# Kernel tuning notes

Hardware: AMD Instinct MI355X
Metric: run time of the kernel (lower is better)

The kernel has to match this reference:

```python
import jax, jax.numpy as jnp
from jax import lax
import numpy as np

GAMMA = 1e-4  # RBF bandwidth (init kwarg gamma)

def setup_inputs() -> dict:
    key = jax.random.key(0)
    ks = jax.random.split(key, 6)
    B, H, W = 2048, 64, 64
    P, D = 4096, 4096  # D = 4 * (H//2) * (W//2)
    NC = 10
    x = jax.random.normal(ks[0], (B, 1, H, W), dtype=jnp.float32)
    prototypes = jax.random.normal(ks[1], (P, D), dtype=jnp.float32) * 0.5
    conv_w = jax.random.normal(ks[2], (4, 1, 2, 2), dtype=jnp.float32) * 0.5
    conv_b = jax.random.normal(ks[3], (4,), dtype=jnp.float32) * 0.1
    head_w = jax.random.normal(ks[4], (NC, P), dtype=jnp.float32) * (1.0 / np.sqrt(P))
    head_b = jax.random.normal(ks[5], (NC,), dtype=jnp.float32) * 0.1
    return {"x": x, "prototypes": prototypes, "conv_w": conv_w,
            "conv_b": conv_b, "head_w": head_w, "head_b": head_b}

def reference(x, prototypes, conv_w, conv_b, head_w, head_b):
    # 2x2 stride-2 conv: [B,1,H,W] -> [B,4,H/2,W/2]
    feats = lax.conv_general_dilated(
        x, conv_w, window_strides=(2, 2), padding="VALID",
        dimension_numbers=("NCHW", "OIHW", "NCHW"))
    feats = feats + conv_b[None, :, None, None]
    B = feats.shape[0]
    feats = feats.reshape(B, -1)  # [B, D]
    # Pairwise squared distance via ||f||^2 + ||p||^2 - 2 f.p (no [B,P,D] blowup)
    f2 = jnp.sum(feats * feats, axis=1, keepdims=True)          # [B,1]
    p2 = jnp.sum(prototypes * prototypes, axis=1)[None, :]      # [1,P]
    d2 = jnp.maximum(f2 + p2 - 2.0 * feats @ prototypes.T, 0.0)  # [B,P]
    kernel_vals = jnp.exp(-GAMMA * d2)
    logits = kernel_vals @ head_w.T + head_b
    return jax.nn.log_softmax(logits, axis=-1)
```

## Files before the change

### kernel.cpp

```cpp
#include <hip/hip_runtime.h>
#include <hip/hip_bf16.h>
#include <stdint.h>

#define GAMMA 1e-4f

typedef int i32x4 __attribute__((ext_vector_type(4)));
typedef int i32x8 __attribute__((ext_vector_type(8)));
typedef float f32x4 __attribute__((ext_vector_type(4)));

__device__ __forceinline__ float bf2f(unsigned short u) {
  unsigned int x = ((unsigned int)u) << 16;
  float f; __builtin_memcpy(&f, &x, 4);
  return f;
}

__device__ __forceinline__ unsigned char f2e4m3(float x) {
  float a = fabsf(x);
  unsigned char s = x < 0.f ? 0x80 : 0;
  a = fminf(a, 448.f);
  if (a < 0.015625f) {
    int q = (int)rintf(a * 512.f);
    return s | (unsigned char)q;
  }
  unsigned int u; __builtin_memcpy(&u, &a, 4);
  u += 0x7FFFFu + ((u >> 20) & 1);
  u &= 0xFFF00000u;
  int e2 = (int)(u >> 23) - 127;
  unsigned int mant = (u >> 20) & 7;
  return s | (unsigned char)(((e2 + 7) << 3) | mant);
}

__device__ __forceinline__ unsigned int pack4(float a, float b, float c, float d) {
  return (unsigned)f2e4m3(a) | ((unsigned)f2e4m3(b) << 8) |
         ((unsigned)f2e4m3(c) << 16) | ((unsigned)f2e4m3(d) << 24);
}

__global__ __launch_bounds__(256) void prep_k(
    const float* __restrict__ x, const float* __restrict__ cw,
    const float* __restrict__ cb, unsigned char* __restrict__ fA8,
    float* __restrict__ f2, const float* __restrict__ pr,
    unsigned char* __restrict__ pB8, float* __restrict__ p2) {
  const int tid = threadIdx.x;
  __shared__ float red[4];
  if (blockIdx.x < 4096) {
    const int j = blockIdx.x;
    const float4* src = (const float4*)(pr + (size_t)j * 4096);
    float ssq = 0.f;
    unsigned int w4[4];
#pragma unroll
    for (int k = 0; k < 4; k++) {
      float4 v = src[tid * 4 + k];
      ssq += v.x * v.x + v.y * v.y + v.z * v.z + v.w * v.w;
      w4[k] = pack4(v.x, v.y, v.z, v.w);
    }
    *(uint4*)(pB8 + (size_t)j * 4096 + tid * 16) = make_uint4(w4[0], w4[1], w4[2], w4[3]);
    for (int off = 32; off > 0; off >>= 1) ssq += __shfl_down(ssq, off);
    if ((tid & 63) == 0) red[tid >> 6] = ssq;
    __syncthreads();
    if (tid == 0) p2[j] = red[0] + red[1] + red[2] + red[3];
  } else {
    const int b = blockIdx.x - 4096;
    __shared__ float swb[20];
    if (tid < 16) swb[tid] = cw[tid];
    else if (tid < 20) swb[tid] = cb[tid - 16];
    __syncthreads();
    float w[16], bias[4];
#pragma unroll
    for (int i = 0; i < 16; i++) w[i] = swb[i];
#pragma unroll
    for (int c = 0; c < 4; c++) bias[c] = swb[16 + c];
    const float* xb = x + (size_t)b * 4096;
    unsigned char* fb8 = fA8 + (size_t)b * 4096;
    const int p0 = tid * 4;
    const int h = p0 >> 5, w0 = p0 & 31;
    const float* r0 = xb + (2 * h) * 64 + 2 * w0;
    const float* r1 = r0 + 64;
    float4 a0 = *(const float4*)r0, a1 = *(const float4*)(r0 + 4);
    float4 c0 = *(const float4*)r1, c1 = *(const float4*)(r1 + 4);
    float ssq = 0.f;
#pragma unroll
    for (int c = 0; c < 4; c++) {
      float w00 = w[c * 4], w01 = w[c * 4 + 1], w10 = w[c * 4 + 2], w11 = w[c * 4 + 3];
      float v0 = bias[c] + a0.x * w00 + a0.y * w01 + c0.x * w10 + c0.y * w11;
      float v1 = bias[c] + a0.z * w00 + a0.w * w01 + c0.z * w10 + c0.w * w11;
      float v2 = bias[c] + a1.x * w00 + a1.y * w01 + c1.x * w10 + c1.y * w11;
      float v3 = bias[c] + a1.z * w00 + a1.w * w01 + c1.z * w10 + c1.w * w11;
      ssq += v0 * v0 + v1 * v1 + v2 * v2 + v3 * v3;
      *(unsigned int*)(fb8 + c * 1024 + p0) = pack4(v0, v1, v2, v3);
    }
    for (int off = 32; off > 0; off >>= 1) ssq += __shfl_down(ssq, off);
    if ((tid & 63) == 0) red[tid >> 6] = ssq;
    __syncthreads();
    if (tid == 0) f2[b] = red[0] + red[1] + red[2] + red[3];
  }
}

#define SWZA(o) ((o) ^ ((((o) >> 12) & 1) << 4))
#define SWZB(o) ((o) ^ ((((o) >> 13) & 1) << 4))
#define TILE_BYTES 49152

#define GLDS(gsrc, ldst)                                                    \
  __builtin_amdgcn_global_load_lds(                                         \
      (__attribute__((address_space(1))) void*)(void*)(gsrc),               \
      (__attribute__((address_space(3))) void*)(ldst), 16, 0, 0)

#define MFMA8(a, b, c)                                                      \
  __builtin_amdgcn_mfma_scale_f32_16x16x128_f8f6f4(                         \
      (a), (b), (c), 0, 0, 0, 0x7f7f7f7fu, 0, 0x7f7f7f7fu)

__device__ __forceinline__ i32x8 read32(const char* p0, const char* p1) {
  i32x4 lo = *(const i32x4*)p0;
  i32x4 hi = *(const i32x4*)p1;
  return __builtin_shufflevector(lo, hi, 0, 1, 2, 3, 4, 5, 6, 7);
}

#define TILE_BODY(PT, DO_STAGE, KB, VMWAIT_CODE)                            \
  {                                                                         \
    i32x8 av0, av1, av2, av3, bv0, bv1, bv2, bv3;                           \
    __builtin_amdgcn_sched_barrier(0);                                      \
    av0 = read32((PT) + arlo[0], (PT) + arhi[0]);                           \
    av1 = read32((PT) + arlo[1], (PT) + arhi[1]);                           \
    av2 = read32((PT) + arlo[2], (PT) + arhi[2]);                           \
    av3 = read32((PT) + arlo[3], (PT) + arhi[3]);                           \
    bv0 = read32((PT) + brlo[0], (PT) + brhi[0]);                           \
    bv1 = read32((PT) + brlo[1], (PT) + brhi[1]);                           \
    __builtin_amdgcn_sched_barrier(0);                                      \
    if (DO_STAGE) {                                                         \
      GLDS(agp[0] + (KB), pt2 + aoff[0]);                                   \
      GLDS(agp[1] + (KB), pt2 + aoff[1]);                                   \
      GLDS(bgp[0] + (KB), pt2 + 16384 + boff[0]);                           \
    }                                                                       \
    bv2 = read32((PT) + brlo[2], (PT) + brhi[2]);                           \
    bv3 = read32((PT) + brlo[3], (PT) + brhi[3]);                           \
    if (DO_STAGE) {                                                         \
      GLDS(bgp[1] + (KB), pt2 + 16384 + boff[1]);                           \
      GLDS(bgp[2] + (KB), pt2 + 16384 + boff[2]);                           \
      GLDS(bgp[3] + (KB), pt2 + 16384 + boff[3]);                           \
    }                                                                       \
    __builtin_amdgcn_sched_barrier(0);                                      \
    asm volatile("s_waitcnt lgkmcnt(4)" ::: "memory");                      \
    __builtin_amdgcn_sched_barrier(0);                                      \
    __builtin_amdgcn_s_setprio(1);                                          \
    acc[0][0] = MFMA8(av0, bv0, acc[0][0]);                                 \
    acc[0][1] = MFMA8(av0, bv1, acc[0][1]);                                 \
    acc[1][0] = MFMA8(av1, bv0, acc[1][0]);                                 \
    acc[1][1] = MFMA8(av1, bv1, acc[1][1]);                                 \
    acc[2][0] = MFMA8(av2, bv0, acc[2][0]);                                 \
    acc[2][1] = MFMA8(av2, bv1, acc[2][1]);                                 \
    acc[3][0] = MFMA8(av3, bv0, acc[3][0]);                                 \
    acc[3][1] = MFMA8(av3, bv1, acc[3][1]);                                 \
    __builtin_amdgcn_s_setprio(0);                                          \
    __builtin_amdgcn_sched_barrier(0);                                      \
    asm volatile("s_waitcnt lgkmcnt(0)" ::: "memory");                      \
    __builtin_amdgcn_sched_barrier(0);                                      \
    __builtin_amdgcn_s_setprio(1);                                          \
    acc[0][2] = MFMA8(av0, bv2, acc[0][2]);                                 \
    acc[0][3] = MFMA8(av0, bv3, acc[0][3]);                                 \
    acc[1][2] = MFMA8(av1, bv2, acc[1][2]);                                 \
    acc[1][3] = MFMA8(av1, bv3, acc[1][3]);                                 \
    acc[2][2] = MFMA8(av2, bv2, acc[2][2]);                                 \
    acc[2][3] = MFMA8(av2, bv3, acc[2][3]);                                 \
    acc[3][2] = MFMA8(av3, bv2, acc[3][2]);                                 \
    acc[3][3] = MFMA8(av3, bv3, acc[3][3]);                                 \
    __builtin_amdgcn_s_setprio(0);                                          \
    VMWAIT_CODE;                                                            \
    __builtin_amdgcn_sched_barrier(0);                                      \
  }

__global__ __launch_bounds__(512, 1) void gemm_kv_k(
    const unsigned char* __restrict__ A, const unsigned char* __restrict__ B,
    const float* __restrict__ f2, const float* __restrict__ p2,
    __hip_bfloat16* __restrict__ kv) {
  __shared__ __align__(16) char lds[3 * TILE_BYTES];
  const int tid = threadIdx.x;
  const int wave = tid >> 6, lane = tid & 63;
  const int q = lane >> 4, l16 = lane & 15;
  const int wr = wave >> 2, wc = wave & 3;

  const int wg = blockIdx.x;
  const int xcd = wg & 7, loc = wg >> 3;
  const int bm = (xcd & 1) * 8 + (loc & 7);
  const int bn = (xcd >> 1) * 4 + (loc >> 3);

  const unsigned char* agp[2];
  const unsigned char* bgp[4];
  int aoff[2], boff[4];
#pragma unroll
  for (int i = 0; i < 2; i++) {
    int phys = (tid + i * 512) * 16;
    aoff[i] = phys;
    int lg = SWZA(phys);
    int kq = lg >> 12, rw = (lg & 4095) >> 5, kl = lg & 31;
    agp[i] = A + (size_t)(bm * 128 + rw) * 4096 + kq * 32 + kl;
  }
#pragma unroll
  for (int i = 0; i < 4; i++) {
    int phys = (tid + i * 512) * 16;
    boff[i] = phys;
    int lg = SWZB(phys);
    int kq = lg >> 13, rw = (lg & 8191) >> 5, kl = lg & 31;
    bgp[i] = B + (size_t)(bn * 256 + rw) * 4096 + kq * 32 + kl;
  }

  int arlo[4], arhi[4], brlo[4], brhi[4];
#pragma unroll
  for (int m = 0; m < 4; m++) {
    int lg = q * 4096 + (wr * 64 + m * 16 + l16) * 32;
    arlo[m] = SWZA(lg);
    arhi[m] = SWZA(lg + 16);
  }
#pragma unroll
  for (int n = 0; n < 4; n++) {
    int lg = q * 8192 + (wc * 64 + n * 16 + l16) * 32;
    brlo[n] = 16384 + SWZB(lg);
    brhi[n] = 16384 + SWZB(lg + 16);
  }

  f32x4 acc[4][4] = {};

  char* pt0 = lds;
  char* pt1 = lds + TILE_BYTES;
  char* pt2 = lds + 2 * TILE_BYTES;

#pragma unroll
  for (int i = 0; i < 2; i++) GLDS(agp[i], pt0 + aoff[i]);
#pragma unroll
  for (int i = 0; i < 4; i++) GLDS(bgp[i], pt0 + 16384 + boff[i]);
#pragma unroll
  for (int i = 0; i < 2; i++) GLDS(agp[i] + 128, pt1 + aoff[i]);
#pragma unroll
  for (int i = 0; i < 4; i++) GLDS(bgp[i] + 128, pt1 + 16384 + boff[i]);
  asm volatile("s_waitcnt vmcnt(6)" ::: "memory");
  __builtin_amdgcn_s_barrier();

#pragma unroll 1
  for (int t = 0; t < 30; ++t) {
    const size_t kb2 = (size_t)(t + 2) * 128;
    TILE_BODY(pt0, 1, kb2,
              asm volatile("s_waitcnt vmcnt(6)" ::: "memory");
              __builtin_amdgcn_sched_barrier(0);
              __builtin_amdgcn_s_barrier());
    char* tmp = pt0; pt0 = pt1; pt1 = pt2; pt2 = tmp;
  }
  TILE_BODY(pt0, 0, 0,
            asm volatile("s_waitcnt vmcnt(0)" ::: "memory");
            __builtin_amdgcn_sched_barrier(0);
            __builtin_amdgcn_s_barrier());
  pt0 = pt1;
  TILE_BODY(pt0, 0, 0, );

  float p2v[4];
#pragma unroll
  for (int n = 0; n < 4; n++) p2v[n] = p2[bn * 256 + wc * 64 + n * 16 + l16];
#pragma unroll
  for (int m = 0; m < 4; m++) {
#pragma unroll
    for (int j = 0; j < 4; j++) {
      int grow = bm * 128 + wr * 64 + m * 16 + q * 4 + j;
      float f2v = f2[grow];
      __hip_bfloat16* kvp = kv + (size_t)grow * 4096 + bn * 256 + wc * 64 + l16;
#pragma unroll
      for (int n = 0; n < 4; n++) {
        float d2 = fmaxf(f2v + p2v[n] - 2.0f * acc[m][n][j], 0.f);
        kvp[n * 16] = __float2bfloat16(__expf(-GAMMA * d2));
      }
    }
  }
}

__global__ __launch_bounds__(256) void head_ls_k(
    const __hip_bfloat16* __restrict__ kv, const float* __restrict__ hw,
    const float* __restrict__ hb, float* __restrict__ out) {
  const int bb = blockIdx.x * 4;
  const int tid = threadIdx.x;
  float part[4][10];
#pragma unroll
  for (int r = 0; r < 4; r++)
#pragma unroll
    for (int c = 0; c < 10; c++) part[r][c] = 0.f;
#pragma unroll
  for (int k = 0; k < 4; k++) {
    int idx = tid + k * 256;
    float4 w[10];
#pragma unroll
    for (int c = 0; c < 10; c++) w[c] = *(const float4*)(hw + c * 4096 + idx * 4);
#pragma unroll
    for (int r = 0; r < 4; r++) {
      ushort4 v = ((const ushort4*)(kv + (size_t)(bb + r) * 4096))[idx];
      float a0 = bf2f(v.x), a1 = bf2f(v.y), a2 = bf2f(v.z), a3 = bf2f(v.w);
#pragma unroll
      for (int c = 0; c < 10; c++)
        part[r][c] += a0 * w[c].x + a1 * w[c].y + a2 * w[c].z + a3 * w[c].w;
    }
  }
#pragma unroll
  for (int r = 0; r < 4; r++)
#pragma unroll
    for (int c = 0; c < 10; c++)
      for (int off = 32; off > 0; off >>= 1) part[r][c] += __shfl_down(part[r][c], off);
  __shared__ float red[4][4][10];
  if ((tid & 63) == 0) {
#pragma unroll
    for (int r = 0; r < 4; r++)
#pragma unroll
      for (int c = 0; c < 10; c++) red[tid >> 6][r][c] = part[r][c];
  }
  __syncthreads();
  if (tid < 4) {
    const int r = tid;
    float l[10], m = -1e30f;
#pragma unroll
    for (int c = 0; c < 10; c++) {
      l[c] = red[0][r][c] + red[1][r][c] + red[2][r][c] + red[3][r][c] + hb[c];
      m = fmaxf(m, l[c]);
    }
    float s = 0.f;
#pragma unroll
    for (int c = 0; c < 10; c++) s += __expf(l[c] - m);
    float lse = logf(s);
#pragma unroll
    for (int c = 0; c < 10; c++) out[(size_t)(bb + r) * 10 + c] = l[c] - m - lse;
  }
}

extern "C" void kernel_launch(void* const* d_in, const int* in_sizes, int n_in,
                              void* d_out, int out_size, void* d_ws, size_t ws_size,
                              hipStream_t stream) {
  const float* x      = (const float*)d_in[0];
  const float* protos = (const float*)d_in[1];
  const float* conv_w = (const float*)d_in[2];
  const float* conv_b = (const float*)d_in[3];
  const float* head_w = (const float*)d_in[4];
  const float* head_b = (const float*)d_in[5];
  float* out = (float*)d_out;
  char* ws = (char*)d_ws;

  unsigned char* pB8  = (unsigned char*)ws;
  unsigned char* fA8  = (unsigned char*)(ws + (16u << 20));
  __hip_bfloat16* kvb = (__hip_bfloat16*)(ws + (24u << 20));
  float* f2 = (float*)(ws + (40u << 20));
  float* p2 = (float*)(ws + (40u << 20) + 8192);

  hipLaunchKernelGGL(prep_k, dim3(6144), dim3(256), 0, stream,
                     x, conv_w, conv_b, fA8, f2, protos, pB8, p2);
  hipLaunchKernelGGL(gemm_kv_k, dim3(256), dim3(512), 0, stream, fA8, pB8, f2, p2, kvb);
  hipLaunchKernelGGL(head_ls_k, dim3(512), dim3(256), 0, stream, kvb, head_w, head_b, out);
}
```

Before: 79.58 us.

## Switch FP8 GEMM to 32x32x64 MFMA with 4-stage ring and register prefetch

Result: slower. 81.84 us (+2.8%).

```diff
diff --git a/kernel.cpp b/kernel.cpp
--- a/kernel.cpp
+++ b/kernel.cpp
@@ -6,7 +6,7 @@
 
 typedef int i32x4 __attribute__((ext_vector_type(4)));
 typedef int i32x8 __attribute__((ext_vector_type(8)));
-typedef float f32x4 __attribute__((ext_vector_type(4)));
+typedef float f32x16 __attribute__((ext_vector_type(16)));
 
 __device__ __forceinline__ float bf2f(unsigned short u) {
   unsigned int x = ((unsigned int)u) << 16;
@@ -97,84 +97,56 @@
 
 #define SWZA(o) ((o) ^ ((((o) >> 12) & 1) << 4))
 #define SWZB(o) ((o) ^ ((((o) >> 13) & 1) << 4))
-#define TILE_BYTES 49152
+#define TILE_BYTES 24576
 
 #define GLDS(gsrc, ldst)                                                    \
   __builtin_amdgcn_global_load_lds(                                         \
       (__attribute__((address_space(1))) void*)(void*)(gsrc),               \
       (__attribute__((address_space(3))) void*)(ldst), 16, 0, 0)
 
-#define MFMA8(a, b, c)                                                      \
-  __builtin_amdgcn_mfma_scale_f32_16x16x128_f8f6f4(                         \
+#define MFMA32(a, b, c)                                                     \
+  __builtin_amdgcn_mfma_scale_f32_32x32x64_f8f6f4(                          \
       (a), (b), (c), 0, 0, 0, 0x7f7f7f7fu, 0, 0x7f7f7f7fu)
 
-__device__ __forceinline__ i32x8 read32(const char* p0, const char* p1) {
-  i32x4 lo = *(const i32x4*)p0;
-  i32x4 hi = *(const i32x4*)p1;
-  return __builtin_shufflevector(lo, hi, 0, 1, 2, 3, 4, 5, 6, 7);
-}
-
-#define TILE_BODY(PT, DO_STAGE, KB, VMWAIT_CODE)                            \
-  {                                                                         \
-    i32x8 av0, av1, av2, av3, bv0, bv1, bv2, bv3;                           \
-    __builtin_amdgcn_sched_barrier(0);                                      \
-    av0 = read32((PT) + arlo[0], (PT) + arhi[0]);                           \
-    av1 = read32((PT) + arlo[1], (PT) + arhi[1]);                           \
-    av2 = read32((PT) + arlo[2], (PT) + arhi[2]);                           \
-    av3 = read32((PT) + arlo[3], (PT) + arhi[3]);                           \
-    bv0 = read32((PT) + brlo[0], (PT) + brhi[0]);                           \
-    bv1 = read32((PT) + brlo[1], (PT) + brhi[1]);                           \
-    __builtin_amdgcn_sched_barrier(0);                                      \
-    if (DO_STAGE) {                                                         \
-      GLDS(agp[0] + (KB), pt2 + aoff[0]);                                   \
-      GLDS(agp[1] + (KB), pt2 + aoff[1]);                                   \
-      GLDS(bgp[0] + (KB), pt2 + 16384 + boff[0]);                           \
-    }                                                                       \
-    bv2 = read32((PT) + brlo[2], (PT) + brhi[2]);                           \
-    bv3 = read32((PT) + brlo[3], (PT) + brhi[3]);                           \
-    if (DO_STAGE) {                                                         \
-      GLDS(bgp[1] + (KB), pt2 + 16384 + boff[1]);                           \
-      GLDS(bgp[2] + (KB), pt2 + 16384 + boff[2]);                           \
-      GLDS(bgp[3] + (KB), pt2 + 16384 + boff[3]);                           \
-    }                                                                       \
-    __builtin_amdgcn_sched_barrier(0);                                      \
-    asm volatile("s_waitcnt lgkmcnt(4)" ::: "memory");                      \
-    __builtin_amdgcn_sched_barrier(0);                                      \
-    __builtin_amdgcn_s_setprio(1);                                          \
-    acc[0][0] = MFMA8(av0, bv0, acc[0][0]);                                 \
-    acc[0][1] = MFMA8(av0, bv1, acc[0][1]);                                 \
-    acc[1][0] = MFMA8(av1, bv0, acc[1][0]);                                 \
-    acc[1][1] = MFMA8(av1, bv1, acc[1][1]);                                 \
-    acc[2][0] = MFMA8(av2, bv0, acc[2][0]);                                 \
-    acc[2][1] = MFMA8(av2, bv1, acc[2][1]);                                 \
-    acc[3][0] = MFMA8(av3, bv0, acc[3][0]);                                 \
-    acc[3][1] = MFMA8(av3, bv1, acc[3][1]);                                 \
-    __builtin_amdgcn_s_setprio(0);                                          \
-    __builtin_amdgcn_sched_barrier(0);                                      \
-    asm volatile("s_waitcnt lgkmcnt(0)" ::: "memory");                      \
-    __builtin_amdgcn_sched_barrier(0);                                      \
-    __builtin_amdgcn_s_setprio(1);                                          \
-    acc[0][2] = MFMA8(av0, bv2, acc[0][2]);                                 \
-    acc[0][3] = MFMA8(av0, bv3, acc[0][3]);                                 \
-    acc[1][2] = MFMA8(av1, bv2, acc[1][2]);                                 \
-    acc[1][3] = MFMA8(av1, bv3, acc[1][3]);                                 \
-    acc[2][2] = MFMA8(av2, bv2, acc[2][2]);                                 \
-    acc[2][3] = MFMA8(av2, bv3, acc[2][3]);                                 \
-    acc[3][2] = MFMA8(av3, bv2, acc[3][2]);                                 \
-    acc[3][3] = MFMA8(av3, bv3, acc[3][3]);                                 \
-    __builtin_amdgcn_s_setprio(0);                                          \
-    VMWAIT_CODE;                                                            \
-    __builtin_amdgcn_sched_barrier(0);                                      \
-  }
+__device__ __forceinline__ i32x8 read32(const char* plo, const char* phi) {
+  i32x8 r;
+  *(i32x4*)&r = *(const i32x4*)plo;
+  *(((i32x4*)&r) + 1) = *(const i32x4*)phi;
+  return r;
+}
+
+#define TBODY(PTN, PTS, CA0, CA1, CB0, CB1, NA0, NA1, NB0, NB1, KB)         \
+  __builtin_amdgcn_sched_barrier(0);                                        \
+  NA0 = read32((PTN) + arlo0, (PTN) + arhi0);                               \
+  NA1 = read32((PTN) + arlo1, (PTN) + arhi1);                               \
+  NB0 = read32((PTN) + brlo0, (PTN) + brhi0);                               \
+  NB1 = read32((PTN) + brlo1, (PTN) + brhi1);                               \
+  __builtin_amdgcn_sched_barrier(0);                                        \
+  GLDS(agp + (KB), (PTS) + aoff);                                           \
+  GLDS(bgp0 + (KB), (PTS) + 8192 + boff0);                                  \
+  GLDS(bgp1 + (KB), (PTS) + 8192 + boff1);                                  \
+  __builtin_amdgcn_sched_barrier(0);                                        \
+  asm volatile("s_waitcnt lgkmcnt(8)" ::: "memory");                        \
+  __builtin_amdgcn_sched_barrier(0);                                        \
+  __builtin_amdgcn_s_setprio(1);                                            \
+  acc00 = MFMA32(CA0, CB0, acc00);                                          \
+  acc01 = MFMA32(CA0, CB1, acc01);                                          \
+  acc10 = MFMA32(CA1, CB0, acc10);                                          \
+  acc11 = MFMA32(CA1, CB1, acc11);                                          \
+  __builtin_amdgcn_s_setprio(0);                                            \
+  __builtin_amdgcn_sched_barrier(0);                                        \
+  asm volatile("s_waitcnt vmcnt(3)" ::: "memory");                          \
+  __builtin_amdgcn_sched_barrier(0);                                        \
+  __builtin_amdgcn_s_barrier();
 
 __global__ __launch_bounds__(512, 1) void gemm_kv_k(
     const unsigned char* __restrict__ A, const unsigned char* __restrict__ B,
     const float* __restrict__ f2, const float* __restrict__ p2,
     __hip_bfloat16* __restrict__ kv) {
-  __shared__ __align__(16) char lds[3 * TILE_BYTES];
+  __shared__ __align__(16) char lds[4 * TILE_BYTES];
   const int tid = threadIdx.x;
   const int wave = tid >> 6, lane = tid & 63;
-  const int q = lane >> 4, l16 = lane & 15;
+  const int h = lane >> 5, l32 = lane & 31;
   const int wr = wave >> 2, wc = wave & 3;
 
   const int wg = blockIdx.x;
@@ -182,90 +154,97 @@
   const int bm = (xcd & 1) * 8 + (loc & 7);
   const int bn = (xcd >> 1) * 4 + (loc >> 3);
 
-  const unsigned char* agp[2];
-  const unsigned char* bgp[4];
-  int aoff[2], boff[4];
-#pragma unroll
-  for (int i = 0; i < 2; i++) {
-    int phys = (tid + i * 512) * 16;
-    aoff[i] = phys;
+  const unsigned char* agp;
+  const unsigned char* bgp0;
+  const unsigned char* bgp1;
+  int aoff, boff0, boff1;
+  {
+    int phys = tid * 16;
+    aoff = phys;
     int lg = SWZA(phys);
-    int kq = lg >> 12, rw = (lg & 4095) >> 5, kl = lg & 31;
-    agp[i] = A + (size_t)(bm * 128 + rw) * 4096 + kq * 32 + kl;
-  }
-#pragma unroll
-  for (int i = 0; i < 4; i++) {
-    int phys = (tid + i * 512) * 16;
-    boff[i] = phys;
+    agp = A + (size_t)(bm * 128 + ((lg & 4095) >> 5)) * 4096 + (lg >> 12) * 32 + (lg & 31);
+  }
+  {
+    int phys = tid * 16;
+    boff0 = phys;
     int lg = SWZB(phys);
-    int kq = lg >> 13, rw = (lg & 8191) >> 5, kl = lg & 31;
-    bgp[i] = B + (size_t)(bn * 256 + rw) * 4096 + kq * 32 + kl;
-  }
-
-  int arlo[4], arhi[4], brlo[4], brhi[4];
-#pragma unroll
-  for (int m = 0; m < 4; m++) {
-    int lg = q * 4096 + (wr * 64 + m * 16 + l16) * 32;
-    arlo[m] = SWZA(lg);
-    arhi[m] = SWZA(lg + 16);
-  }
-#pragma unroll
-  for (int n = 0; n < 4; n++) {
-    int lg = q * 8192 + (wc * 64 + n * 16 + l16) * 32;
-    brlo[n] = 16384 + SWZB(lg);
-    brhi[n] = 16384 + SWZB(lg + 16);
-  }
-
-  f32x4 acc[4][4] = {};
+    bgp0 = B + (size_t)(bn * 256 + ((lg & 8191) >> 5)) * 4096 + (lg >> 13) * 32 + (lg & 31);
+  }
+  {
+    int phys = (tid + 512) * 16;
+    boff1 = phys;
+    int lg = SWZB(phys);
+    bgp1 = B + (size_t)(bn * 256 + ((lg & 8191) >> 5)) * 4096 + (lg >> 13) * 32 + (lg & 31);
+  }
+
+  const int lgA0 = h * 4096 + (wr * 64 + l32) * 32;
+  const int lgA1 = h * 4096 + (wr * 64 + 32 + l32) * 32;
+  const int lgB0 = h * 8192 + (wc * 64 + l32) * 32;
+  const int lgB1 = h * 8192 + (wc * 64 + 32 + l32) * 32;
+  const int arlo0 = SWZA(lgA0), arhi0 = SWZA(lgA0 + 16);
+  const int arlo1 = SWZA(lgA1), arhi1 = SWZA(lgA1 + 16);
+  const int brlo0 = 8192 + SWZB(lgB0), brhi0 = 8192 + SWZB(lgB0 + 16);
+  const int brlo1 = 8192 + SWZB(lgB1), brhi1 = 8192 + SWZB(lgB1 + 16);
+
+  f32x16 acc00 = {}, acc01 = {}, acc10 = {}, acc11 = {};
+  i32x8 Xa0, Xa1, Xb0, Xb1, Ya0, Ya1, Yb0, Yb1;
 
   char* pt0 = lds;
   char* pt1 = lds + TILE_BYTES;
   char* pt2 = lds + 2 * TILE_BYTES;
-
-#pragma unroll
-  for (int i = 0; i < 2; i++) GLDS(agp[i], pt0 + aoff[i]);
-#pragma unroll
-  for (int i = 0; i < 4; i++) GLDS(bgp[i], pt0 + 16384 + boff[i]);
-#pragma unroll
-  for (int i = 0; i < 2; i++) GLDS(agp[i] + 128, pt1 + aoff[i]);
-#pragma unroll
-  for (int i = 0; i < 4; i++) GLDS(bgp[i] + 128, pt1 + 16384 + boff[i]);
-  asm volatile("s_waitcnt vmcnt(6)" ::: "memory");
+  char* pt3 = lds + 3 * TILE_BYTES;
+
+  GLDS(agp, pt0 + aoff);
+  GLDS(bgp0, pt0 + 8192 + boff0);
+  GLDS(bgp1, pt0 + 8192 + boff1);
+  GLDS(agp + 64, pt1 + aoff);
+  GLDS(bgp0 + 64, pt1 + 8192 + boff0);
+  GLDS(bgp1 + 64, pt1 + 8192 + boff1);
+  GLDS(agp + 128, pt2 + aoff);
+  GLDS(bgp0 + 128, pt2 + 8192 + boff0);
+  GLDS(bgp1 + 128, pt2 + 8192 + boff1);
+  asm volatile("s_waitcnt vmcnt(3)" ::: "memory");
   __builtin_amdgcn_s_barrier();
 
+  Xa0 = read32(pt0 + arlo0, pt0 + arhi0);
+  Xa1 = read32(pt0 + arlo1, pt0 + arhi1);
+  Xb0 = read32(pt0 + brlo0, pt0 + brhi0);
+  Xb1 = read32(pt0 + brlo1, pt0 + brhi1);
+
 #pragma unroll 1
-  for (int t = 0; t < 30; ++t) {
-    const size_t kb2 = (size_t)(t + 2) * 128;
-    TILE_BODY(pt0, 1, kb2,
-              asm volatile("s_waitcnt vmcnt(6)" ::: "memory");
-              __builtin_amdgcn_sched_barrier(0);
-              __builtin_amdgcn_s_barrier());
-    char* tmp = pt0; pt0 = pt1; pt1 = pt2; pt2 = tmp;
-  }
-  TILE_BODY(pt0, 0, 0,
-            asm volatile("s_waitcnt vmcnt(0)" ::: "memory");
-            __builtin_amdgcn_sched_barrier(0);
-            __builtin_amdgcn_s_barrier());
-  pt0 = pt1;
-  TILE_BODY(pt0, 0, 0, );
-
-  float p2v[4];
-#pragma unroll
-  for (int n = 0; n < 4; n++) p2v[n] = p2[bn * 256 + wc * 64 + n * 16 + l16];
-#pragma unroll
-  for (int m = 0; m < 4; m++) {
-#pragma unroll
-    for (int j = 0; j < 4; j++) {
-      int grow = bm * 128 + wr * 64 + m * 16 + q * 4 + j;
-      float f2v = f2[grow];
-      __hip_bfloat16* kvp = kv + (size_t)grow * 4096 + bn * 256 + wc * 64 + l16;
-#pragma unroll
-      for (int n = 0; n < 4; n++) {
-        float d2 = fmaxf(f2v + p2v[n] - 2.0f * acc[m][n][j], 0.f);
-        kvp[n * 16] = __float2bfloat16(__expf(-GAMMA * d2));
-      }
-    }
-  }
+  for (int t = 0; t < 64; t += 2) {
+    const int kb1 = ((t + 3) & 63) * 64;
+    const int kb2 = ((t + 4) & 63) * 64;
+    TBODY(pt1, pt3, Xa0, Xa1, Xb0, Xb1, Ya0, Ya1, Yb0, Yb1, kb1);
+    TBODY(pt2, pt0, Ya0, Ya1, Yb0, Yb1, Xa0, Xa1, Xb0, Xb1, kb2);
+    char* s0 = pt0; char* s1 = pt1;
+    pt0 = pt2; pt1 = pt3; pt2 = s0; pt3 = s1;
+  }
+
+  asm volatile("s_waitcnt vmcnt(0) lgkmcnt(0)" ::: "memory");
+
+  const int colb = bn * 256 + wc * 64 + l32;
+  const float p2v0 = p2[colb];
+  const float p2v1 = p2[colb + 32];
+
+#define EPI(ACC0, ACC1, MOFF)                                               \
+  {                                                                         \
+    const int rb = bm * 128 + wr * 64 + (MOFF) + 4 * h;                     \
+    _Pragma("unroll") for (int g = 0; g < 4; g++) {                         \
+      _Pragma("unroll") for (int j = 0; j < 4; j++) {                       \
+        const int grow = rb + j + 8 * g;                                    \
+        const float f2v = f2[grow];                                         \
+        __hip_bfloat16* kvp = kv + (size_t)grow * 4096 + colb;              \
+        float d0 = fmaxf(f2v + p2v0 - 2.0f * ACC0[4 * g + j], 0.f);         \
+        float d1 = fmaxf(f2v + p2v1 - 2.0f * ACC1[4 * g + j], 0.f);         \
+        kvp[0] = __float2bfloat16(__expf(-GAMMA * d0));                     \
+        kvp[32] = __float2bfloat16(__expf(-GAMMA * d1));                    \
+      }                                                                     \
+    }                                                                       \
+  }
+  EPI(acc00, acc01, 0)
+  EPI(acc10, acc11, 32)
+#undef EPI
 }
 
 __global__ __launch_bounds__(256) void head_ls_k(
```

## Shrink GEMM tile to 128x128 with double-buffering and two blocks per CU

Applied to the files above, without the earlier changes.

New measurement: 92.04 us. +15.7%, slower.

```diff
diff --git a/kernel.cpp b/kernel.cpp
--- a/kernel.cpp
+++ b/kernel.cpp
@@ -95,9 +95,8 @@
   }
 }
 
-#define SWZA(o) ((o) ^ ((((o) >> 12) & 1) << 4))
-#define SWZB(o) ((o) ^ ((((o) >> 13) & 1) << 4))
-#define TILE_BYTES 49152
+#define SWZ(o) ((o) ^ ((((o) >> 12) & 1) << 4))
+#define TILE_BYTES 32768
 
 #define GLDS(gsrc, ldst)                                                    \
   __builtin_amdgcn_global_load_lds(                                         \
@@ -114,29 +113,27 @@
   return __builtin_shufflevector(lo, hi, 0, 1, 2, 3, 4, 5, 6, 7);
 }
 
-#define TILE_BODY(PT, DO_STAGE, KB, VMWAIT_CODE)                            \
+#define TBODY(CUR, NXT, KB)                                                 \
   {                                                                         \
     i32x8 av0, av1, av2, av3, bv0, bv1, bv2, bv3;                           \
     __builtin_amdgcn_sched_barrier(0);                                      \
-    av0 = read32((PT) + arlo[0], (PT) + arhi[0]);                           \
-    av1 = read32((PT) + arlo[1], (PT) + arhi[1]);                           \
-    av2 = read32((PT) + arlo[2], (PT) + arhi[2]);                           \
-    av3 = read32((PT) + arlo[3], (PT) + arhi[3]);                           \
-    bv0 = read32((PT) + brlo[0], (PT) + brhi[0]);                           \
-    bv1 = read32((PT) + brlo[1], (PT) + brhi[1]);                           \
-    __builtin_amdgcn_sched_barrier(0);                                      \
-    if (DO_STAGE) {                                                         \
-      GLDS(agp[0] + (KB), pt2 + aoff[0]);                                   \
-      GLDS(agp[1] + (KB), pt2 + aoff[1]);                                   \
-      GLDS(bgp[0] + (KB), pt2 + 16384 + boff[0]);                           \
-    }                                                                       \
-    bv2 = read32((PT) + brlo[2], (PT) + brhi[2]);                           \
-    bv3 = read32((PT) + brlo[3], (PT) + brhi[3]);                           \
-    if (DO_STAGE) {                                                         \
-      GLDS(bgp[1] + (KB), pt2 + 16384 + boff[1]);                           \
-      GLDS(bgp[2] + (KB), pt2 + 16384 + boff[2]);                           \
-      GLDS(bgp[3] + (KB), pt2 + 16384 + boff[3]);                           \
-    }                                                                       \
+    av0 = read32((CUR) + arlo[0], (CUR) + arhi[0]);                         \
+    av1 = read32((CUR) + arlo[1], (CUR) + arhi[1]);                         \
+    av2 = read32((CUR) + arlo[2], (CUR) + arhi[2]);                         \
+    av3 = read32((CUR) + arlo[3], (CUR) + arhi[3]);                         \
+    bv0 = read32((CUR) + brlo[0], (CUR) + brhi[0]);                         \
+    bv1 = read32((CUR) + brlo[1], (CUR) + brhi[1]);                         \
+    __builtin_amdgcn_sched_barrier(0);                                      \
+    GLDS(agp[0] + (KB), (NXT) + aoff[0]);                                   \
+    GLDS(agp[1] + (KB), (NXT) + aoff[1]);                                   \
+    GLDS(agp[2] + (KB), (NXT) + aoff[2]);                                   \
+    GLDS(agp[3] + (KB), (NXT) + aoff[3]);                                   \
+    bv2 = read32((CUR) + brlo[2], (CUR) + brhi[2]);                         \
+    bv3 = read32((CUR) + brlo[3], (CUR) + brhi[3]);                         \
+    GLDS(bgp[0] + (KB), (NXT) + 16384 + boff[0]);                           \
+    GLDS(bgp[1] + (KB), (NXT) + 16384 + boff[1]);                           \
+    GLDS(bgp[2] + (KB), (NXT) + 16384 + boff[2]);                           \
+    GLDS(bgp[3] + (KB), (NXT) + 16384 + boff[3]);                           \
     __builtin_amdgcn_sched_barrier(0);                                      \
     asm volatile("s_waitcnt lgkmcnt(4)" ::: "memory");                      \
     __builtin_amdgcn_sched_barrier(0);                                      \
@@ -163,102 +160,85 @@
     acc[3][2] = MFMA8(av3, bv2, acc[3][2]);                                 \
     acc[3][3] = MFMA8(av3, bv3, acc[3][3]);                                 \
     __builtin_amdgcn_s_setprio(0);                                          \
-    VMWAIT_CODE;                                                            \
-    __builtin_amdgcn_sched_barrier(0);                                      \
-  }
-
-__global__ __launch_bounds__(512, 1) void gemm_kv_k(
+    __builtin_amdgcn_sched_barrier(0);                                      \
+    asm volatile("s_waitcnt vmcnt(0)" ::: "memory");                        \
+    __builtin_amdgcn_sched_barrier(0);                                      \
+    __builtin_amdgcn_s_barrier();                                           \
+  }
+
+__global__ __launch_bounds__(256, 2) void gemm_kv_k(
     const unsigned char* __restrict__ A, const unsigned char* __restrict__ B,
     const float* __restrict__ f2, const float* __restrict__ p2,
     __hip_bfloat16* __restrict__ kv) {
-  __shared__ __align__(16) char lds[3 * TILE_BYTES];
+  __shared__ __align__(16) char lds[2 * TILE_BYTES];
   const int tid = threadIdx.x;
   const int wave = tid >> 6, lane = tid & 63;
   const int q = lane >> 4, l16 = lane & 15;
-  const int wr = wave >> 2, wc = wave & 3;
+  const int wr = wave >> 1, wc = wave & 1;
 
   const int wg = blockIdx.x;
   const int xcd = wg & 7, loc = wg >> 3;
-  const int bm = (xcd & 1) * 8 + (loc & 7);
-  const int bn = (xcd >> 1) * 4 + (loc >> 3);
-
-  const unsigned char* agp[2];
+  const int bm = loc >> 2;
+  const int bn = xcd * 4 + (loc & 3);
+
+  const unsigned char* agp[4];
   const unsigned char* bgp[4];
-  int aoff[2], boff[4];
-#pragma unroll
-  for (int i = 0; i < 2; i++) {
-    int phys = (tid + i * 512) * 16;
+  int aoff[4], boff[4];
+#pragma unroll
+  for (int i = 0; i < 4; i++) {
+    int phys = (tid + i * 256) * 16;
     aoff[i] = phys;
-    int lg = SWZA(phys);
+    boff[i] = phys;
+    int lg = SWZ(phys);
     int kq = lg >> 12, rw = (lg & 4095) >> 5, kl = lg & 31;
     agp[i] = A + (size_t)(bm * 128 + rw) * 4096 + kq * 32 + kl;
-  }
-#pragma unroll
-  for (int i = 0; i < 4; i++) {
-    int phys = (tid + i * 512) * 16;
-    boff[i] = phys;
-    int lg = SWZB(phys);
-    int kq = lg >> 13, rw = (lg & 8191) >> 5, kl = lg & 31;
-    bgp[i] = B + (size_t)(bn * 256 + rw) * 4096 + kq * 32 + kl;
+    bgp[i] = B + (size_t)(bn * 128 + rw) * 4096 + kq * 32 + kl;
   }
 
   int arlo[4], arhi[4], brlo[4], brhi[4];
 #pragma unroll
   for (int m = 0; m < 4; m++) {
     int lg = q * 4096 + (wr * 64 + m * 16 + l16) * 32;
-    arlo[m] = SWZA(lg);
-    arhi[m] = SWZA(lg + 16);
+    arlo[m] = SWZ(lg);
+    arhi[m] = SWZ(lg + 16);
   }
 #pragma unroll
   for (int n = 0; n < 4; n++) {
-    int lg = q * 8192 + (wc * 64 + n * 16 + l16) * 32;
-    brlo[n] = 16384 + SWZB(lg);
-    brhi[n] = 16384 + SWZB(lg + 16);
+    int lg = q * 4096 + (wc * 64 + n * 16 + l16) * 32;
+    brlo[n] = 16384 + SWZ(lg);
+    brhi[n] = 16384 + SWZ(lg + 16);
   }
 
   f32x4 acc[4][4] = {};
 
-  char* pt0 = lds;
-  char* pt1 = lds + TILE_BYTES;
-  char* pt2 = lds + 2 * TILE_BYTES;
-
-#pragma unroll
-  for (int i = 0; i < 2; i++) GLDS(agp[i], pt0 + aoff[i]);
-#pragma unroll
-  for (int i = 0; i < 4; i++) GLDS(bgp[i], pt0 + 16384 + boff[i]);
-#pragma unroll
-  for (int i = 0; i < 2; i++) GLDS(agp[i] + 128, pt1 + aoff[i]);
-#pragma unroll
-  for (int i = 0; i < 4; i++) GLDS(bgp[i] + 128, pt1 + 16384 + boff[i]);
-  asm volatile("s_waitcnt vmcnt(6)" ::: "memory");
+  char* buf0 = lds;
+  char* buf1 = lds + TILE_BYTES;
+
+#pragma unroll
+  for (int i = 0; i < 4; i++) GLDS(agp[i], buf0 + aoff[i]);
+#pragma unroll
+  for (int i = 0; i < 4; i++) GLDS(bgp[i], buf0 + 16384 + boff[i]);
+  asm volatile("s_waitcnt vmcnt(0)" ::: "memory");
   __builtin_amdgcn_s_barrier();
 
 #pragma unroll 1
-  for (int t = 0; t < 30; ++t) {
-    const size_t kb2 = (size_t)(t + 2) * 128;
-    TILE_BODY(pt0, 1, kb2,
-              asm volatile("s_waitcnt vmcnt(6)" ::: "memory");
-              __builtin_amdgcn_sched_barrier(0);
-              __builtin_amdgcn_s_barrier());
-    char* tmp = pt0; pt0 = pt1; pt1 = pt2; pt2 = tmp;
-  }
-  TILE_BODY(pt0, 0, 0,
-            asm volatile("s_waitcnt vmcnt(0)" ::: "memory");
-            __builtin_amdgcn_sched_barrier(0);
-            __builtin_amdgcn_s_barrier());
-  pt0 = pt1;
-  TILE_BODY(pt0, 0, 0, );
+  for (int t = 0; t < 32; t += 2) {
+    const int kb1 = ((t + 1) & 31) * 128;
+    const int kb2 = ((t + 2) & 31) * 128;
+    TBODY(buf0, buf1, kb1);
+    TBODY(buf1, buf0, kb2);
+  }
 
   float p2v[4];
 #pragma unroll
-  for (int n = 0; n < 4; n++) p2v[n] = p2[bn * 256 + wc * 64 + n * 16 + l16];
+  for (int n = 0; n < 4; n++) p2v[n] = p2[bn * 128 + wc * 64 + n * 16 + l16];
 #pragma unroll
   for (int m = 0; m < 4; m++) {
 #pragma unroll
     for (int j = 0; j < 4; j++) {
       int grow = bm * 128 + wr * 64 + m * 16 + q * 4 + j;
       float f2v = f2[grow];
-      __hip_bfloat16* kvp = kv + (size_t)grow * 4096 + bn * 256 + wc * 64 + l16;
+      __hip_bfloat16* kvp = kv + (size_t)grow * 4096 + bn * 128 + wc * 64 + l16;
 #pragma unroll
       for (int n = 0; n < 4; n++) {
         float d2 = fmaxf(f2v + p2v[n] - 2.0f * acc[m][n][j], 0.f);
@@ -271,11 +251,11 @@
 __global__ __launch_bounds__(256) void head_ls_k(
     const __hip_bfloat16* __restrict__ kv, const float* __restrict__ hw,
     const float* __restrict__ hb, float* __restrict__ out) {
-  const int bb = blockIdx.x * 4;
+  const int bb = blockIdx.x * 8;
   const int tid = threadIdx.x;
-  float part[4][10];
-#pragma unroll
-  for (int r = 0; r < 4; r++)
+  float part[8][10];
+#pragma unroll
+  for (int r = 0; r < 8; r++)
 #pragma unroll
     for (int c = 0; c < 10; c++) part[r][c] = 0.f;
 #pragma unroll
@@ -285,7 +265,7 @@
 #pragma unroll
     for (int c = 0; c < 10; c++) w[c] = *(const float4*)(hw + c * 4096 + idx * 4);
 #pragma unroll
-    for (int r = 0; r < 4; r++) {
+    for (int r = 0; r < 8; r++) {
       ushort4 v = ((const ushort4*)(kv + (size_t)(bb + r) * 4096))[idx];
       float a0 = bf2f(v.x), a1 = bf2f(v.y), a2 = bf2f(v.z), a3 = bf2f(v.w);
 #pragma unroll
@@ -294,19 +274,19 @@
     }
   }
 #pragma unroll
-  for (int r = 0; r < 4; r++)
+  for (int r = 0; r < 8; r++)
 #pragma unroll
     for (int c = 0; c < 10; c++)
       for (int off = 32; off > 0; off >>= 1) part[r][c] += __shfl_down(part[r][c], off);
-  __shared__ float red[4][4][10];
+  __shared__ float red[4][8][10];
   if ((tid & 63) == 0) {
 #pragma unroll
-    for (int r = 0; r < 4; r++)
+    for (int r = 0; r < 8; r++)
 #pragma unroll
       for (int c = 0; c < 10; c++) red[tid >> 6][r][c] = part[r][c];
   }
   __syncthreads();
-  if (tid < 4) {
+  if (tid < 8) {
     const int r = tid;
     float l[10], m = -1e30f;
 #pragma unroll
@@ -343,6 +323,6 @@
 
   hipLaunchKernelGGL(prep_k, dim3(6144), dim3(256), 0, stream,
                      x, conv_w, conv_b, fA8, f2, protos, pB8, p2);
-  hipLaunchKernelGGL(gemm_kv_k, dim3(256), dim3(512), 0, stream, fA8, pB8, f2, p2, kvb);
-  hipLaunchKernelGGL(head_ls_k, dim3(512), dim3(256), 0, stream, kvb, head_w, head_b, out);
-}
+  hipLaunchKernelGGL(gemm_kv_k, dim3(512), dim3(256), 0, stream, fA8, pB8, f2, p2, kvb);
+  hipLaunchKernelGGL(head_ls_k, dim3(256), dim3(256), 0, stream, kvb, head_w, head_b, out);
+}
```
